# Kernel tuning notes

Hardware: AMD Instinct MI355X
Metric: run time of the kernel (lower is better)

## Reference

```python
import jax, jax.numpy as jnp
import numpy as np

B, H, W, EMB = 8, 128, 128, 6
NF = 256  # number_of_filters


def setup_inputs() -> dict:
    key = jax.random.key(0)
    ks = jax.random.split(key, 12)
    s = 0.02  # init_func-style small normal init
    image = jax.random.normal(ks[0], (B, 1, H, W), jnp.float32)
    mask_embedding = jax.random.normal(ks[1], (B, EMB, H, W), jnp.float32)
    # conv stack: 134->256 (s2), 256->512 (s2), 512->1024 (s2), 1024->1024 (s2), avgpool8, 1024->128 (1x1)
    w0 = jax.random.normal(ks[2], (NF, W + EMB, 4, 4), jnp.float32) * s
    b0 = jnp.zeros((NF,), jnp.float32)
    w1 = jax.random.normal(ks[3], (2 * NF, NF, 4, 4), jnp.float32) * s
    b1 = jnp.zeros((2 * NF,), jnp.float32)
    w2 = jax.random.normal(ks[4], (4 * NF, 2 * NF, 4, 4), jnp.float32) * s
    b2 = jnp.zeros((4 * NF,), jnp.float32)
    w3 = jax.random.normal(ks[5], (4 * NF, 4 * NF, 4, 4), jnp.float32) * s
    b3 = jnp.zeros((4 * NF,), jnp.float32)
    w4 = jax.random.normal(ks[6], (W, 4 * NF, 1, 1), jnp.float32) * s
    b4 = jnp.zeros((W,), jnp.float32)
    return dict(image=image, mask_embedding=mask_embedding,
                w0=w0, b0=b0, w1=w1, b1=b1, w2=w2, b2=b2, w3=w3, b3=b3, w4=w4, b4=b4)


def _spectral_map(image, mask_embedding):
    # Original: kspace = fft2(image); for each column i zero out all other k-space
    # columns, ifft2 (unnormalized torch.ifft => 1/(H*W)), take real part.
    # Since only column i is nonzero, ifft2 separates:
    #   sep[b,i,h,w] = Re( (1/W) * ifft_H(kspace[:, :, i])[h] * exp(2j*pi*w*i/W) )
    Bv, _, Hv, Wv = image.shape
    kspace = jnp.fft.fft2(image[:, 0])                    # (B, H, W) complex64
    col = jnp.fft.ifft(kspace, axis=1) / Wv               # (B, H, W_i); ifft over height gives 1/H
    idx = jnp.arange(Wv)
    twiddle = jnp.exp((2j * jnp.pi / Wv) * jnp.outer(idx, idx).astype(jnp.float32))  # (W_spatial, W_i) complex64
    sep = jnp.real(jnp.einsum('bhi,wi->bihw', col, twiddle))  # (B, W, H, W) float32
    return jnp.concatenate([sep, mask_embedding], axis=1)     # (B, W+EMB, H, W)


def _conv(x, w, b, stride):
    y = jax.lax.conv_general_dilated(x, w, (stride, stride), [(1, 1), (1, 1)],
                                     dimension_numbers=('NCHW', 'OIHW', 'NCHW'))
    return y + b[None, :, None, None]


def _inorm(x):  # InstanceNorm2d, affine=False, eps=1e-5
    m = jnp.mean(x, (2, 3), keepdims=True)
    v = jnp.var(x, (2, 3), keepdims=True)
    return (x - m) * jax.lax.rsqrt(v + 1e-5)


def _lrelu(x):
    return jax.nn.leaky_relu(x, 0.2)


def reference(image, mask_embedding, w0, b0, w1, b1, w2, b2, w3, b3, w4, b4):
    x = _spectral_map(image, mask_embedding)       # (B, 134, 128, 128)
    x = _lrelu(_conv(x, w0, b0, 2))                # (B, 256, 64, 64)
    x = _lrelu(_inorm(_conv(x, w1, b1, 2)))        # (B, 512, 32, 32)
    x = _lrelu(_inorm(_conv(x, w2, b2, 2)))        # (B, 1024, 16, 16)
    x = _lrelu(_inorm(_conv(x, w3, b3, 2)))        # (B, 1024, 8, 8)
    pooled = jnp.mean(x, (2, 3))                   # AvgPool(k=8) -> (B, 1024)
    out = jnp.einsum('bc,oc->bo', pooled, w4[:, :, 0, 0]) + b4  # 1x1 conv + squeeze -> (B, 128)
    return out
```

## Files before the change

kernel.cpp:

```cpp
#include <hip/hip_runtime.h>
#include <hip/hip_bf16.h>
#include <cstdint>
#include <cstddef>

typedef __attribute__((ext_vector_type(8))) short bf16x8;
typedef __attribute__((ext_vector_type(4))) float f32x4;

#define PI2F 6.283185307179586f

__device__ __forceinline__ float bf2f(unsigned short u) {
  union { float f; uint32_t i; } x; x.i = ((uint32_t)u) << 16; return x.f;
}
__device__ __forceinline__ unsigned short f2bf(float f) {
  union { float f; uint32_t i; } x; x.f = f;
  uint32_t r = x.i + 0x7FFF + ((x.i >> 16) & 1);
  return (unsigned short)(r >> 16);
}

__global__ void dft_kernel(const float* __restrict__ img, float2* __restrict__ col,
                           float2* __restrict__ tw) {
  __shared__ float row[128];
  __shared__ float2 twl[128];
  const int bh = blockIdx.x;
  const int i = threadIdx.x;
  row[i] = img[bh * 128 + i];
  float s, c;
  sincosf(PI2F * (float)i / 128.0f, &s, &c);
  twl[i] = make_float2(c, s);
  __syncthreads();
  if (bh == 0) tw[i] = twl[i];
  float sr = 0.f, si = 0.f;
  for (int w = 0; w < 128; ++w) {
    float v = row[w];
    float2 t = twl[(i * w) & 127];
    sr += v * t.x;
    si -= v * t.y;
  }
  col[bh * 128 + i] = make_float2(sr * (1.0f / 128.0f), si * (1.0f / 128.0f));
}

__global__ __launch_bounds__(256)
void sep_cl_kernel(const float2* __restrict__ col, const float2* __restrict__ tw,
                   const float* __restrict__ maskE, unsigned short* __restrict__ x0) {
  __shared__ unsigned short lt[128][132];
  __shared__ float2 twl[128];
  const int bh = blockIdx.x;
  const int b = bh >> 7, h = bh & 127;
  const int tid = threadIdx.x;
  if (tid < 128) twl[tid] = tw[tid];
  __syncthreads();
  {
    const int c = tid >> 1;
    const int w0 = (tid & 1) * 64;
    float2 cv = col[(b * 128 + h) * 128 + c];
#pragma unroll 8
    for (int j = 0; j < 64; ++j) {
      int w = w0 + j;
      float2 t = twl[(w * c) & 127];
      lt[c][w] = f2bf(cv.x * t.x - cv.y * t.y);
    }
  }
  __syncthreads();
  if (tid < 144) {
    const int c = tid;
    unsigned short* dst = x0 + ((size_t)bh * 128) * 144 + c;
    if (c < 128) {
      for (int w = 0; w < 128; ++w) dst[(size_t)w * 144] = lt[c][w];
    } else if (c < 134) {
      const float* m = maskE + ((size_t)(b * 6 + (c - 128)) * 128 + h) * 128;
      for (int w = 0; w < 128; ++w) dst[(size_t)w * 144] = f2bf(m[w]);
    } else {
      for (int w = 0; w < 128; ++w) dst[(size_t)w * 144] = 0;
    }
  }
}

template<int CIN, int CINP>
__global__ __launch_bounds__(256)
void cvtperm_kernel(const float* __restrict__ src, unsigned short* __restrict__ dst) {
  __shared__ unsigned short tile[16][68];
  const int m = blockIdx.y;
  const int ci0 = blockIdx.x * 64;
  const int tid = threadIdx.x;
  {
    const int ci = ci0 + (tid >> 2);
    const int t0 = (tid & 3) * 4;
    float4 v = make_float4(0.f, 0.f, 0.f, 0.f);
    if (ci < CIN) v = *reinterpret_cast<const float4*>(&src[((size_t)m * CIN + ci) * 16 + t0]);
    const int cr = tid >> 2;
    tile[t0 + 0][cr] = f2bf(v.x);
    tile[t0 + 1][cr] = f2bf(v.y);
    tile[t0 + 2][cr] = f2bf(v.z);
    tile[t0 + 3][cr] = f2bf(v.w);
  }
  __syncthreads();
  {
    const int t = tid >> 4;
    const int co = (tid & 15) * 4;
    const int ci = ci0 + co;
    if (ci < CINP) {
      ushort4 o;
      o.x = tile[t][co]; o.y = tile[t][co + 1]; o.z = tile[t][co + 2]; o.w = tile[t][co + 3];
      *reinterpret_cast<ushort4*>(&dst[(size_t)m * (16 * CINP) + (size_t)t * CINP + ci]) = o;
    }
  }
}

template<int CINP, int CSTOR, int COUT, int HI, int WI, int HO, int WO, int NSPLIT, bool FUSED>
__global__ __launch_bounds__(256, 2)
void conv_cl3_kernel(const unsigned short* __restrict__ X,
                     const unsigned short* __restrict__ Wt,
                     const float* __restrict__ bias,
                     unsigned short* __restrict__ Y,
                     float* __restrict__ P) {
  constexpr int KTOT = 16 * CINP;
  constexpr int CPT = CINP / 32;
  constexpr int HOWO = HO * WO;
  constexpr int LHW = __builtin_ctz(HOWO);
  constexpr int LWO = __builtin_ctz(WO);
  constexpr int TPS = 16 / NSPLIT;
  constexpr size_t PSTRIDE = (size_t)8 * HOWO * COUT;
  constexpr int NIT = TPS * CPT;

  __shared__ __align__(16) unsigned short As[2][128 * 32];
  __shared__ __align__(16) unsigned short Bs[2][128 * 32];

  const int tid = threadIdx.x;
  const int lane = tid & 63;
  const int wv = tid >> 6;
  const int wm = wv >> 1, wn = wv & 1;
  const int n0 = blockIdx.x * 128;
  const int m0 = blockIdx.y * 128;
  const int split = blockIdx.z;
  const int r = lane & 15, g = lane >> 4;

  const int row0 = tid >> 2;
  const int row1 = row0 + 64;
  const int chk = tid & 3;
  const int lw0 = row0 * 32 + (((chk + ((row0 >> 1) & 3)) & 3) * 8);
  const int lw1 = row1 * 32 + (((chk + ((row1 >> 1) & 3)) & 3) * 8);

  int bb0, bho0, bwo0, bb1, bho1, bwo1;
  {
    int rn0 = n0 + row0, rn1 = n0 + row1;
    bb0 = rn0 >> LHW; bb1 = rn1 >> LHW;
    int re0 = rn0 & (HOWO - 1), re1 = rn1 & (HOWO - 1);
    bho0 = re0 >> LWO; bho1 = re1 >> LWO;
    bwo0 = re0 & (WO - 1); bwo1 = re1 & (WO - 1);
  }

  const int tap0 = split * TPS;
  int tapI = tap0, ccI = 0;
  size_t boff0, boff1; bool bok0, bok1;
  auto tap_geom = [&](int t) {
    int kh = t >> 2, kw = t & 3;
    {
      int h = 2 * bho0 - 1 + kh, w = 2 * bwo0 - 1 + kw;
      bool hv = (unsigned)h < (unsigned)HI, wvv = (unsigned)w < (unsigned)WI;
      bok0 = hv && wvv;
      boff0 = (((size_t)bb0 * HI + (hv ? h : 0)) * WI + (wvv ? w : 0)) * (size_t)CSTOR;
    }
    {
      int h = 2 * bho1 - 1 + kh, w = 2 * bwo1 - 1 + kw;
      bool hv = (unsigned)h < (unsigned)HI, wvv = (unsigned)w < (unsigned)WI;
      bok1 = hv && wvv;
      boff1 = (((size_t)bb1 * HI + (hv ? h : 0)) * WI + (wvv ? w : 0)) * (size_t)CSTOR;
    }
  };
  tap_geom(tapI);

  auto issue = [&](uint4& a0r, uint4& a1r, uint4& b0r, uint4& b1r) {
    const int kbase = tapI * CINP + ccI * 32 + chk * 8;
    a0r = *reinterpret_cast<const uint4*>(Wt + (size_t)(m0 + row0) * KTOT + kbase);
    a1r = *reinterpret_cast<const uint4*>(Wt + (size_t)(m0 + row1) * KTOT + kbase);
    int ci = ccI * 32 + chk * 8;
    bool ok0 = bok0, ok1 = bok1;
    int cic = ci;
    if constexpr (CSTOR < CINP) {
      if (ci >= CSTOR) { ok0 = false; ok1 = false; cic = 0; }
    }
    uint4 z = make_uint4(0u, 0u, 0u, 0u);
    uint4 v0 = *reinterpret_cast<const uint4*>(X + boff0 + cic);
    uint4 v1 = *reinterpret_cast<const uint4*>(X + boff1 + cic);
    b0r = ok0 ? v0 : z;
    b1r = ok1 ? v1 : z;
  };
  auto advance = [&]() {
    ccI++;
    if (ccI == CPT) { ccI = 0; tapI++; if (tapI < tap0 + TPS) tap_geom(tapI); }
  };

  uint4 avA0, avA1, bvA0, bvA1;
  uint4 avB0, avB1, bvB0, bvB1;
  issue(avA0, avA1, bvA0, bvA1); advance();
  issue(avB0, avB1, bvB0, bvB1); advance();

  f32x4 acc[4][4] = {};

#define CONV_PHASE(BUF, AV0, AV1, BV0, BV1, HASNEXT)                                    \
  *reinterpret_cast<uint4*>(&As[BUF][lw0]) = AV0;                                       \
  *reinterpret_cast<uint4*>(&As[BUF][lw1]) = AV1;                                       \
  *reinterpret_cast<uint4*>(&Bs[BUF][lw0]) = BV0;                                       \
  *reinterpret_cast<uint4*>(&Bs[BUF][lw1]) = BV1;                                       \
  __syncthreads();                                                                      \
  if (HASNEXT) { issue(AV0, AV1, BV0, BV1); advance(); }                                \
  {                                                                                     \
    bf16x8 af[4], bf[4];                                                                \
    _Pragma("unroll")                                                                   \
    for (int mi = 0; mi < 4; ++mi) {                                                    \
      int rw = wm * 64 + mi * 16 + r;                                                   \
      af[mi] = *reinterpret_cast<const bf16x8*>(                                        \
          &As[BUF][rw * 32 + (((g + ((rw >> 1) & 3)) & 3) * 8)]);                       \
    }                                                                                   \
    _Pragma("unroll")                                                                   \
    for (int ni = 0; ni < 4; ++ni) {                                                    \
      int rw = wn * 64 + ni * 16 + r;                                                   \
      bf[ni] = *reinterpret_cast<const bf16x8*>(                                        \
          &Bs[BUF][rw * 32 + (((g + ((rw >> 1) & 3)) & 3) * 8)]);                       \
    }                                                                                   \
    _Pragma("unroll")                                                                   \
    for (int mi = 0; mi < 4; ++mi)                                                      \
      _Pragma("unroll")                                                                 \
      for (int ni = 0; ni < 4; ++ni)                                                    \
        acc[mi][ni] = __builtin_amdgcn_mfma_f32_16x16x32_bf16(af[mi], bf[ni],           \
                                                              acc[mi][ni], 0, 0, 0);    \
  }

  for (int ii = 0; ii < NIT / 2; ++ii) {
    CONV_PHASE(0, avA0, avA1, bvA0, bvA1, (2 * ii + 2 < NIT))
    CONV_PHASE(1, avB0, avB1, bvB0, bvB1, (2 * ii + 3 < NIT))
  }
#undef CONV_PHASE

#pragma unroll
  for (int ni = 0; ni < 4; ++ni) {
    int n = n0 + wn * 64 + ni * 16 + r;
    int b = n >> LHW;
    int rem = n & (HOWO - 1);
    size_t obase = ((size_t)b * HOWO + rem) * COUT;
#pragma unroll
    for (int mi = 0; mi < 4; ++mi) {
      int mb = m0 + wm * 64 + mi * 16 + g * 4;
      f32x4 a = acc[mi][ni];
      if constexpr (FUSED) {
        float v0 = a[0] + bias[mb + 0]; v0 = v0 > 0.f ? v0 : 0.2f * v0;
        float v1 = a[1] + bias[mb + 1]; v1 = v1 > 0.f ? v1 : 0.2f * v1;
        float v2 = a[2] + bias[mb + 2]; v2 = v2 > 0.f ? v2 : 0.2f * v2;
        float v3 = a[3] + bias[mb + 3]; v3 = v3 > 0.f ? v3 : 0.2f * v3;
        ushort4 o;
        o.x = f2bf(v0); o.y = f2bf(v1); o.z = f2bf(v2); o.w = f2bf(v3);
        *reinterpret_cast<ushort4*>(&Y[obase + mb]) = o;
      } else {
        *reinterpret_cast<float4*>(&P[split * PSTRIDE + obase + mb]) =
            make_float4(a[0], a[1], a[2], a[3]);
      }
    }
  }
}

template<int HOWO, int COUT, int NSPLIT>
__global__ __launch_bounds__(256)
void inorm_cl3_kernel(const float* __restrict__ P, unsigned short* __restrict__ Y) {
  constexpr int PER = HOWO / 32;
  constexpr size_t PSTRIDE = (size_t)8 * HOWO * COUT;
  const int b = blockIdx.y;
  const int cl = threadIdx.x & 7;
  const int c = blockIdx.x * 8 + cl;
  const int hw0 = threadIdx.x >> 3;
  const float* base = P + ((size_t)b * HOWO) * COUT + c;
  float v[PER];
  float s1 = 0.f, s2 = 0.f;
#pragma unroll
  for (int j = 0; j < PER; ++j) {
    int hw = hw0 + j * 32;
    float x = 0.f;
#pragma unroll
    for (int s = 0; s < NSPLIT; ++s) x += base[s * PSTRIDE + (size_t)hw * COUT];
    v[j] = x; s1 += x; s2 += x * x;
  }
  __shared__ float r1[32][9], r2[32][9];
  __shared__ float ms[8], rs[8];
  r1[hw0][cl] = s1; r2[hw0][cl] = s2;
  __syncthreads();
  if (threadIdx.x < 8) {
    float a1 = 0.f, a2 = 0.f;
#pragma unroll
    for (int i = 0; i < 32; ++i) { a1 += r1[i][threadIdx.x]; a2 += r2[i][threadIdx.x]; }
    float mean = a1 * (1.0f / HOWO);
    float var = a2 * (1.0f / HOWO) - mean * mean;
    ms[threadIdx.x] = mean;
    rs[threadIdx.x] = rsqrtf(var + 1e-5f);
  }
  __syncthreads();
  const float mean = ms[cl], rstd = rs[cl];
  unsigned short* yb = Y + ((size_t)b * HOWO) * COUT + c;
#pragma unroll
  for (int j = 0; j < PER; ++j) {
    int hw = hw0 + j * 32;
    float t = (v[j] - mean) * rstd;
    t = t > 0.f ? t : 0.2f * t;
    yb[(size_t)hw * COUT] = f2bf(t);
  }
}

__global__ __launch_bounds__(256)
void pool_cl_kernel(const unsigned short* __restrict__ X, float* __restrict__ pooled) {
  const int b = blockIdx.x;
  const int c4 = threadIdx.x * 4;
  float4 acc = make_float4(0.f, 0.f, 0.f, 0.f);
  for (int hw = 0; hw < 64; ++hw) {
    ushort4 v = *reinterpret_cast<const ushort4*>(&X[((size_t)b * 64 + hw) * 1024 + c4]);
    acc.x += bf2f(v.x); acc.y += bf2f(v.y); acc.z += bf2f(v.z); acc.w += bf2f(v.w);
  }
  acc.x *= (1.0f / 64.0f); acc.y *= (1.0f / 64.0f);
  acc.z *= (1.0f / 64.0f); acc.w *= (1.0f / 64.0f);
  *reinterpret_cast<float4*>(&pooled[b * 1024 + c4]) = acc;
}

__global__ __launch_bounds__(64)
void fc_kernel(const float* __restrict__ pooled, const float* __restrict__ w4,
               const float* __restrict__ b4, float* __restrict__ out) {
  const int bo = blockIdx.x;
  const int b = bo >> 7, o = bo & 127;
  const int lane = threadIdx.x;
  float s = 0.f;
#pragma unroll
  for (int j = 0; j < 16; ++j) {
    int c = lane + j * 64;
    s += pooled[b * 1024 + c] * w4[o * 1024 + c];
  }
#pragma unroll
  for (int off = 32; off > 0; off >>= 1) s += __shfl_xor(s, off);
  if (lane == 0) out[bo] = s + b4[o];
}

extern "C" void kernel_launch(void* const* d_in, const int* in_sizes, int n_in,
                              void* d_out, int out_size, void* d_ws, size_t ws_size,
                              hipStream_t stream) {
  (void)in_sizes; (void)n_in; (void)out_size; (void)ws_size;
  const float* image = (const float*)d_in[0];
  const float* maskE = (const float*)d_in[1];
  const float* w0 = (const float*)d_in[2];
  const float* b0 = (const float*)d_in[3];
  const float* w1 = (const float*)d_in[4];
  const float* w2 = (const float*)d_in[6];
  const float* w3 = (const float*)d_in[8];
  const float* w4 = (const float*)d_in[10];
  const float* b4 = (const float*)d_in[11];
  float* out = (float*)d_out;

  char* ws = (char*)d_ws;
  size_t off = 0;
  auto alloc = [&](size_t bytes) -> void* {
    void* p = ws + off;
    off = (off + bytes + 255) & ~(size_t)255;
    return p;
  };

  unsigned short* wbuf = (unsigned short*)alloc((size_t)1024 * 16384 * 2);
  char* bufA = (char*)alloc((size_t)8 * 128 * 128 * 144 * 2);
  char* bufB = (char*)alloc((size_t)8 * 4096 * 256 * 2);
  float2* col = (float2*)alloc((size_t)131072 * sizeof(float2));
  float2* tw = (float2*)alloc(128 * sizeof(float2));
  float* pooled = (float*)alloc(8192 * 4);

  unsigned short* x0 = (unsigned short*)bufA;
  float* part = (float*)bufA;
  unsigned short* a0 = (unsigned short*)bufB;
  unsigned short* a1 = (unsigned short*)bufB;
  unsigned short* a2 = (unsigned short*)bufB;
  unsigned short* a3 = (unsigned short*)bufB;

  dft_kernel<<<1024, 128, 0, stream>>>(image, col, tw);
  sep_cl_kernel<<<1024, 256, 0, stream>>>(col, tw, maskE, x0);

  cvtperm_kernel<134, 160><<<dim3(3, 256), 256, 0, stream>>>(w0, wbuf);
  conv_cl3_kernel<160, 144, 256, 128, 128, 64, 64, 1, true>
      <<<dim3(256, 2, 1), 256, 0, stream>>>(x0, wbuf, b0, a0, nullptr);

  cvtperm_kernel<256, 256><<<dim3(4, 512), 256, 0, stream>>>(w1, wbuf);
  conv_cl3_kernel<256, 256, 512, 64, 64, 32, 32, 2, false>
      <<<dim3(64, 4, 2), 256, 0, stream>>>(a0, wbuf, nullptr, nullptr, part);
  inorm_cl3_kernel<1024, 512, 2><<<dim3(64, 8), 256, 0, stream>>>(part, a1);

  cvtperm_kernel<512, 512><<<dim3(8, 1024), 256, 0, stream>>>(w2, wbuf);
  conv_cl3_kernel<512, 512, 1024, 32, 32, 16, 16, 4, false>
      <<<dim3(16, 8, 4), 256, 0, stream>>>(a1, wbuf, nullptr, nullptr, part);
  inorm_cl3_kernel<256, 1024, 4><<<dim3(128, 8), 256, 0, stream>>>(part, a2);

  cvtperm_kernel<1024, 1024><<<dim3(16, 1024), 256, 0, stream>>>(w3, wbuf);
  conv_cl3_kernel<1024, 1024, 1024, 16, 16, 8, 8, 16, false>
      <<<dim3(4, 8, 16), 256, 0, stream>>>(a2, wbuf, nullptr, nullptr, part);
  inorm_cl3_kernel<64, 1024, 16><<<dim3(128, 8), 256, 0, stream>>>(part, a3);

  pool_cl_kernel<<<8, 256, 0, stream>>>(a3, pooled);
  fc_kernel<<<1024, 64, 0, stream>>>(pooled, w4, b4, out);
}
```

Measured before the change: 316.1 us.

## Rewrite spectral layout kernel, store split-K partials as bf16, double split counts

The spectral separation kernel now writes channel-contiguous vectorized rows directly instead of staging a transpose in shared memory and doing strided scalar stores. The conv kernel's split-K partition moves from whole taps to channel chunks, so it can use more splits, and the split counts for layers 1-3 are doubled to fill more CUs. Split-K partial sums are stored as bf16 instead of fp32 to halve partial-buffer traffic. Rounding each partial to bf16 before the instance-norm reduction adds numerical error.

```diff
diff --git a/kernel.cpp b/kernel.cpp
--- a/kernel.cpp
+++ b/kernel.cpp
@@ -40,38 +40,49 @@
 }
 
 __global__ __launch_bounds__(256)
-void sep_cl_kernel(const float2* __restrict__ col, const float2* __restrict__ tw,
-                   const float* __restrict__ maskE, unsigned short* __restrict__ x0) {
-  __shared__ unsigned short lt[128][132];
+void sep_cl2_kernel(const float2* __restrict__ col, const float2* __restrict__ tw,
+                    const float* __restrict__ maskE, unsigned short* __restrict__ x0) {
+  __shared__ float2 cl[128];
   __shared__ float2 twl[128];
   const int bh = blockIdx.x;
   const int b = bh >> 7, h = bh & 127;
   const int tid = threadIdx.x;
-  if (tid < 128) twl[tid] = tw[tid];
+  if (tid < 128) {
+    cl[tid] = col[(b * 128 + h) * 128 + tid];
+    twl[tid] = tw[tid];
+  }
   __syncthreads();
-  {
-    const int c = tid >> 1;
-    const int w0 = (tid & 1) * 64;
-    float2 cv = col[(b * 128 + h) * 128 + c];
-#pragma unroll 8
-    for (int j = 0; j < 64; ++j) {
-      int w = w0 + j;
-      float2 t = twl[(w * c) & 127];
-      lt[c][w] = f2bf(cv.x * t.x - cv.y * t.y);
-    }
-  }
-  __syncthreads();
-  if (tid < 144) {
-    const int c = tid;
-    unsigned short* dst = x0 + ((size_t)bh * 128) * 144 + c;
-    if (c < 128) {
-      for (int w = 0; w < 128; ++w) dst[(size_t)w * 144] = lt[c][w];
-    } else if (c < 134) {
-      const float* m = maskE + ((size_t)(b * 6 + (c - 128)) * 128 + h) * 128;
-      for (int w = 0; w < 128; ++w) dst[(size_t)w * 144] = f2bf(m[w]);
-    } else {
-      for (int w = 0; w < 128; ++w) dst[(size_t)w * 144] = 0;
-    }
+  const int p = tid >> 1;
+  const int c0 = (tid & 1) * 64;
+  unsigned short* dst = x0 + ((size_t)bh * 128 + p) * 144;
+#pragma unroll
+  for (int j = 0; j < 16; ++j) {
+    ushort4 o;
+#pragma unroll
+    for (int q = 0; q < 4; ++q) {
+      int c = c0 + 4 * j + q;
+      float2 cv = cl[c];
+      float2 t = twl[(p * c) & 127];
+      float v = cv.x * t.x - cv.y * t.y;
+      ((unsigned short*)&o)[q] = f2bf(v);
+    }
+    *reinterpret_cast<ushort4*>(dst + c0 + 4 * j) = o;
+  }
+  if (tid < 128) {
+    const int w = tid;
+    float v[6];
+#pragma unroll
+    for (int cm = 0; cm < 6; ++cm)
+      v[cm] = maskE[(((size_t)(b * 6 + cm) * 128) + h) * 128 + w];
+    unsigned short* d2 = x0 + ((size_t)bh * 128 + w) * 144 + 128;
+    ushort4 m0, m1, mz;
+    m0.x = f2bf(v[0]); m0.y = f2bf(v[1]); m0.z = f2bf(v[2]); m0.w = f2bf(v[3]);
+    m1.x = f2bf(v[4]); m1.y = f2bf(v[5]); m1.z = 0; m1.w = 0;
+    mz.x = 0; mz.y = 0; mz.z = 0; mz.w = 0;
+    reinterpret_cast<ushort4*>(d2)[0] = m0;
+    reinterpret_cast<ushort4*>(d2)[1] = m1;
+    reinterpret_cast<ushort4*>(d2)[2] = mz;
+    reinterpret_cast<ushort4*>(d2)[3] = mz;
   }
 }
 
@@ -108,19 +119,20 @@
 
 template<int CINP, int CSTOR, int COUT, int HI, int WI, int HO, int WO, int NSPLIT, bool FUSED>
 __global__ __launch_bounds__(256, 2)
-void conv_cl3_kernel(const unsigned short* __restrict__ X,
+void conv_cl9_kernel(const unsigned short* __restrict__ X,
                      const unsigned short* __restrict__ Wt,
                      const float* __restrict__ bias,
                      unsigned short* __restrict__ Y,
-                     float* __restrict__ P) {
+                     unsigned short* __restrict__ P) {
   constexpr int KTOT = 16 * CINP;
   constexpr int CPT = CINP / 32;
+  constexpr int NCHT = 16 * CPT;
+  constexpr int CPS = NCHT / NSPLIT;
   constexpr int HOWO = HO * WO;
   constexpr int LHW = __builtin_ctz(HOWO);
   constexpr int LWO = __builtin_ctz(WO);
-  constexpr int TPS = 16 / NSPLIT;
   constexpr size_t PSTRIDE = (size_t)8 * HOWO * COUT;
-  constexpr int NIT = TPS * CPT;
+  constexpr int NIT = CPS;
 
   __shared__ __align__(16) unsigned short As[2][128 * 32];
   __shared__ __align__(16) unsigned short Bs[2][128 * 32];
@@ -149,8 +161,8 @@
     bwo0 = re0 & (WO - 1); bwo1 = re1 & (WO - 1);
   }
 
-  const int tap0 = split * TPS;
-  int tapI = tap0, ccI = 0;
+  const int start = split * CPS;
+  int tapI = start / CPT, ccI = start % CPT;
   size_t boff0, boff1; bool bok0, bok1;
   auto tap_geom = [&](int t) {
     int kh = t >> 2, kw = t & 3;
@@ -187,7 +199,7 @@
   };
   auto advance = [&]() {
     ccI++;
-    if (ccI == CPT) { ccI = 0; tapI++; if (tapI < tap0 + TPS) tap_geom(tapI); }
+    if (ccI == CPT) { ccI = 0; tapI++; if (tapI < 16) tap_geom(tapI); }
   };
 
   uint4 avA0, avA1, bvA0, bvA1;
@@ -251,8 +263,9 @@
         o.x = f2bf(v0); o.y = f2bf(v1); o.z = f2bf(v2); o.w = f2bf(v3);
         *reinterpret_cast<ushort4*>(&Y[obase + mb]) = o;
       } else {
-        *reinterpret_cast<float4*>(&P[split * PSTRIDE + obase + mb]) =
-            make_float4(a[0], a[1], a[2], a[3]);
+        ushort4 o;
+        o.x = f2bf(a[0]); o.y = f2bf(a[1]); o.z = f2bf(a[2]); o.w = f2bf(a[3]);
+        *reinterpret_cast<ushort4*>(&P[split * PSTRIDE + obase + mb]) = o;
       }
     }
   }
@@ -260,14 +273,14 @@
 
 template<int HOWO, int COUT, int NSPLIT>
 __global__ __launch_bounds__(256)
-void inorm_cl3_kernel(const float* __restrict__ P, unsigned short* __restrict__ Y) {
+void inorm_bf_kernel(const unsigned short* __restrict__ P, unsigned short* __restrict__ Y) {
   constexpr int PER = HOWO / 32;
   constexpr size_t PSTRIDE = (size_t)8 * HOWO * COUT;
   const int b = blockIdx.y;
   const int cl = threadIdx.x & 7;
   const int c = blockIdx.x * 8 + cl;
   const int hw0 = threadIdx.x >> 3;
-  const float* base = P + ((size_t)b * HOWO) * COUT + c;
+  const unsigned short* base = P + ((size_t)b * HOWO) * COUT + c;
   float v[PER];
   float s1 = 0.f, s2 = 0.f;
 #pragma unroll
@@ -275,7 +288,7 @@
     int hw = hw0 + j * 32;
     float x = 0.f;
 #pragma unroll
-    for (int s = 0; s < NSPLIT; ++s) x += base[s * PSTRIDE + (size_t)hw * COUT];
+    for (int s = 0; s < NSPLIT; ++s) x += bf2f(base[s * PSTRIDE + (size_t)hw * COUT]);
     v[j] = x; s1 += x; s2 += x * x;
   }
   __shared__ float r1[32][9], r2[32][9];
@@ -357,41 +370,42 @@
     return p;
   };
 
+  const size_t X0BYTES = (size_t)8 * 128 * 128 * 144 * 2;
   unsigned short* wbuf = (unsigned short*)alloc((size_t)1024 * 16384 * 2);
-  char* bufA = (char*)alloc((size_t)8 * 128 * 128 * 144 * 2);
+  char* bufA = (char*)alloc(X0BYTES + 256);
   char* bufB = (char*)alloc((size_t)8 * 4096 * 256 * 2);
   float2* col = (float2*)alloc((size_t)131072 * sizeof(float2));
   float2* tw = (float2*)alloc(128 * sizeof(float2));
   float* pooled = (float*)alloc(8192 * 4);
 
   unsigned short* x0 = (unsigned short*)bufA;
-  float* part = (float*)bufA;
+  unsigned short* part = (unsigned short*)bufA;
   unsigned short* a0 = (unsigned short*)bufB;
   unsigned short* a1 = (unsigned short*)bufB;
   unsigned short* a2 = (unsigned short*)bufB;
   unsigned short* a3 = (unsigned short*)bufB;
 
   dft_kernel<<<1024, 128, 0, stream>>>(image, col, tw);
-  sep_cl_kernel<<<1024, 256, 0, stream>>>(col, tw, maskE, x0);
+  sep_cl2_kernel<<<1024, 256, 0, stream>>>(col, tw, maskE, x0);
 
   cvtperm_kernel<134, 160><<<dim3(3, 256), 256, 0, stream>>>(w0, wbuf);
-  conv_cl3_kernel<160, 144, 256, 128, 128, 64, 64, 1, true>
+  conv_cl9_kernel<160, 144, 256, 128, 128, 64, 64, 1, true>
       <<<dim3(256, 2, 1), 256, 0, stream>>>(x0, wbuf, b0, a0, nullptr);
 
   cvtperm_kernel<256, 256><<<dim3(4, 512), 256, 0, stream>>>(w1, wbuf);
-  conv_cl3_kernel<256, 256, 512, 64, 64, 32, 32, 2, false>
-      <<<dim3(64, 4, 2), 256, 0, stream>>>(a0, wbuf, nullptr, nullptr, part);
-  inorm_cl3_kernel<1024, 512, 2><<<dim3(64, 8), 256, 0, stream>>>(part, a1);
+  conv_cl9_kernel<256, 256, 512, 64, 64, 32, 32, 4, false>
+      <<<dim3(64, 4, 4), 256, 0, stream>>>(a0, wbuf, nullptr, nullptr, part);
+  inorm_bf_kernel<1024, 512, 4><<<dim3(64, 8), 256, 0, stream>>>(part, a1);
 
   cvtperm_kernel<512, 512><<<dim3(8, 1024), 256, 0, stream>>>(w2, wbuf);
-  conv_cl3_kernel<512, 512, 1024, 32, 32, 16, 16, 4, false>
-      <<<dim3(16, 8, 4), 256, 0, stream>>>(a1, wbuf, nullptr, nullptr, part);
-  inorm_cl3_kernel<256, 1024, 4><<<dim3(128, 8), 256, 0, stream>>>(part, a2);
+  conv_cl9_kernel<512, 512, 1024, 32, 32, 16, 16, 8, false>
+      <<<dim3(16, 8, 8), 256, 0, stream>>>(a1, wbuf, nullptr, nullptr, part);
+  inorm_bf_kernel<256, 1024, 8><<<dim3(128, 8), 256, 0, stream>>>(part, a2);
 
   cvtperm_kernel<1024, 1024><<<dim3(16, 1024), 256, 0, stream>>>(w3, wbuf);
-  conv_cl3_kernel<1024, 1024, 1024, 16, 16, 8, 8, 16, false>
-      <<<dim3(4, 8, 16), 256, 0, stream>>>(a2, wbuf, nullptr, nullptr, part);
-  inorm_cl3_kernel<64, 1024, 16><<<dim3(128, 8), 256, 0, stream>>>(part, a3);
+  conv_cl9_kernel<1024, 1024, 1024, 16, 16, 8, 8, 32, false>
+      <<<dim3(4, 8, 32), 256, 0, stream>>>(a2, wbuf, nullptr, nullptr, part);
+  inorm_bf_kernel<64, 1024, 32><<<dim3(128, 8), 256, 0, stream>>>(part, a3);
 
   pool_cl_kernel<<<8, 256, 0, stream>>>(a3, pooled);
   fc_kernel<<<1024, 64, 0, stream>>>(pooled, w4, b4, out);
```

New measurement: 383.4 us. 1.21x slower.
